# Performance work log

Measured on AMD Instinct MI355X. Metric: run time of the kernel, lower is better.

The kernel has to match this reference:

```python
import jax, jax.numpy as jnp
import numpy as np

D = 1024      # embed_dim
H = 1365      # expert_hidden_dim = int(4096 / (select_top_k + num_shared_experts)) = int(4096/3)
E = 7         # num_experts = base_num_experts*factor - num_shared = 8 - 1
K = 2         # select_top_k
S_EXP = 1     # num_shared_experts
ALPHA = 0.01
C_Z = 0.001


def setup_inputs() -> dict:
    key = jax.random.key(0)
    ks = jax.random.split(key, 8)
    scaled = lambda k, shape, fan: jax.random.normal(k, shape, jnp.float32) * (1.0 / np.sqrt(fan))
    return {
        "x": jax.random.normal(ks[0], (4, 512, D), jnp.float32),
        "Wg": scaled(ks[1], (E, D), D),            # router weight (no bias)
        "W1": scaled(ks[2], (E, H, D), D),          # routed experts ffn[0] weight
        "b1": jnp.zeros((E, H), jnp.float32),
        "W2": scaled(ks[3], (E, D, H), H),          # routed experts ffn[3] weight
        "b2": jnp.zeros((E, D), jnp.float32),
        "Ws1": scaled(ks[4], (S_EXP, H, D), D),     # shared experts
        "bs1": jnp.zeros((S_EXP, H), jnp.float32),
        "Ws2": scaled(ks[5], (S_EXP, D, H), H),
        "bs2": jnp.zeros((S_EXP, D), jnp.float32),
    }


def _moe_forward(x, Wg, W1, b1, W2, b2, Ws1, bs1, Ws2, bs2):
    B, S, _ = x.shape
    xf = x.reshape(-1, D)                               # [N, D] flattened tokens
    N = xf.shape[0]

    # Gate (eval mode: no router noise, no dropout)
    logits = jnp.einsum('nd,ed->ne', xf, Wg)            # [N, E]
    dense_gate = jax.nn.softmax(logits, axis=-1)
    topk_logits, topk_idx = jax.lax.top_k(logits, K)    # [N, K]
    topk_w = jax.nn.softmax(topk_logits, axis=-1)       # [N, K]

    # Dense gate matrix: weight for selected experts, 0 elsewhere (equivalent to
    # the sorted dispatch + per-expert FFN + index_add combine in the original).
    gates = jnp.zeros((N, E), xf.dtype).at[jnp.arange(N)[:, None], topk_idx].set(topk_w)

    # Routed experts: exact GELU (approximate='none')
    h = jax.nn.gelu(jnp.einsum('nd,ehd->enh', xf, W1) + b1[:, None, :], approximate=False)  # [E, N, H]
    y = jnp.einsum('enh,edh->end', h, W2) + b2[:, None, :]                                  # [E, N, D]
    routed = jnp.einsum('ne,end->nd', gates, y)                                             # [N, D]

    # Shared experts (applied to every token, summed)
    hs = jax.nn.gelu(jnp.einsum('nd,shd->snh', xf, Ws1) + bs1[:, None, :], approximate=False)
    shared = jnp.einsum('snh,sdh->nd', hs, Ws2) + bs2.sum(0)

    final = (routed + shared).reshape(B, S, D)

    # Aux losses
    counts = jnp.zeros((E,), jnp.float32).at[topk_idx.reshape(-1)].add(1.0)  # bincount (non-diff, like torch long)
    dispatch_fraction = jax.lax.stop_gradient(counts) / (N * K)
    l_aux = ALPHA * E * jnp.sum(dispatch_fraction * dense_gate.mean(axis=0))
    cz_lz = C_Z * jnp.mean(jax.nn.logsumexp(logits, axis=-1) ** 2)
    return final, l_aux, cz_lz


def reference(x, Wg, W1, b1, W2, b2, Ws1, bs1, Ws2, bs2):
    return _moe_forward(x, Wg, W1, b1, W2, b2, Ws1, bs1, Ws2, bs2)
```

## Files before the change

kernel.cpp:

```cpp
#include <hip/hip_runtime.h>
#include <hip/hip_bf16.h>
#include <math.h>

typedef unsigned short u16;
typedef __attribute__((ext_vector_type(8))) short bf16x8;
typedef __attribute__((ext_vector_type(16))) float f32x16;

constexpr int D_ = 1024;
constexpr int H_ = 1365;
constexpr int E_ = 7;
constexpr int NTOK = 2048;
constexpr int HP = 1408;
constexpr int NE = 8;
constexpr int SHARED_BASE = 4096;
constexpr int SLOTS = 6144;

#define CI_COUNT 0
#define CI_OFF   8

constexpr size_t WS_CTRL = 0;
constexpr size_t WS_TIDX = 256;
constexpr size_t WS_TW   = WS_TIDX + (size_t)NTOK*2*4;
constexpr size_t WS_PROB = WS_TW   + (size_t)NTOK*2*4;
constexpr size_t WS_LSE2 = WS_PROB + (size_t)NTOK*8*4;
constexpr size_t WS_STOK = WS_LSE2 + (size_t)NTOK*4;
constexpr size_t WS_SW   = WS_STOK + (size_t)SLOTS*4;
constexpr size_t WS_B1   = WS_SW   + (size_t)SLOTS*4;
constexpr size_t WS_B2   = WS_B1   + (size_t)NE*H_*4;
constexpr size_t WS_XB   = ((WS_B2 + (size_t)NE*D_*4) + 255) & ~(size_t)255;
constexpr size_t WS_W1B  = WS_XB  + (size_t)NTOK*D_*2;
constexpr size_t WS_W2B  = WS_W1B + (size_t)NE*H_*D_*2;
constexpr size_t WS_HEB  = WS_W2B + (size_t)NE*D_*HP*2;

__device__ __forceinline__ u16 f2bf(float f) {
    __hip_bfloat16 h = __float2bfloat16(f);
    return __builtin_bit_cast(u16, h);
}

__device__ __forceinline__ void gload_lds16(const u16* g, u16* l) {
    __builtin_amdgcn_global_load_lds(
        (const __attribute__((address_space(1))) void*)g,
        (__attribute__((address_space(3))) void*)l, 16, 0, 0);
}

__device__ __forceinline__ uint4 pack8(float4 a, float4 b) {
    union { u16 h[8]; uint4 v; } u;
    u.h[0]=f2bf(a.x); u.h[1]=f2bf(a.y); u.h[2]=f2bf(a.z); u.h[3]=f2bf(a.w);
    u.h[4]=f2bf(b.x); u.h[5]=f2bf(b.y); u.h[6]=f2bf(b.z); u.h[7]=f2bf(b.w);
    return u.v;
}

__device__ __forceinline__ float fast_gelu(float v) {
    float u = 0.7978845608f * v * (1.f + 0.044715f * v * v);
    float e = __expf(2.f * u);
    float t = 1.f - 2.f / (e + 1.f);
    return 0.5f * v * (1.f + t);
}

#define BM 128
#define BN 128
#define KSTEP 64
#define ATILE (BM*KSTEP)

#define MFMA32(a,b,c) __builtin_amdgcn_mfma_f32_32x32x16_bf16(a, b, c, 0, 0, 0)

template<bool USE_STOK>
__device__ __forceinline__ void gemm1_body(u16* As, u16* Bs,
    const u16* xb, const u16* w1e, const float* b1e,
    const int* stok, int offset, int m0, int valid, int nt,
    u16* heb)
{
    int t = threadIdx.x, wid = t >> 6, lane = t & 63;
    int rl = lane >> 3, cl = lane & 7;
    int sg = cl ^ rl;

    const u16* aP[2]; const u16* bP[2]; int dOff[2];
    #pragma unroll
    for (int c = 0; c < 2; c++) {
        int row = wid*16 + c*8 + rl;
        int ar = min(row, valid-1);
        int tok = USE_STOK ? stok[offset + m0 + ar] : (m0 + ar);
        aP[c] = xb + (size_t)tok*D_ + sg*8;
        int jg = min(nt*BN + row, H_-1);
        bP[c] = w1e + (size_t)jg*D_ + sg*8;
        dOff[c] = (wid*16 + c*8)*KSTEP;
    }

    int wm = (wid >> 2)*64, wn = (wid & 3)*32;
    int fr = lane & 31, hi = lane >> 5, f7 = lane & 7;
    f32x16 acc[2] = {};

    #pragma unroll
    for (int c = 0; c < 2; c++) {
        gload_lds16(aP[c], As + dOff[c]);
        gload_lds16(bP[c], Bs + dOff[c]);
    }
    constexpr int nIter = D_/KSTEP;
    int cur = 0;
    for (int tt = 0; tt < nIter; ++tt) {
        if (tt + 1 < nIter) {
            int bo2 = (cur^1)*ATILE;
            int ko = (tt+1)*KSTEP;
            #pragma unroll
            for (int c = 0; c < 2; c++) {
                gload_lds16(aP[c]+ko, As + bo2 + dOff[c]);
                gload_lds16(bP[c]+ko, Bs + bo2 + dOff[c]);
            }
            asm volatile("s_waitcnt vmcnt(4)" ::: "memory");
        } else {
            asm volatile("s_waitcnt vmcnt(0)" ::: "memory");
        }
        __builtin_amdgcn_s_barrier();
        __builtin_amdgcn_sched_barrier(0);
        const u16* ab = As + cur*ATILE;
        const u16* bb = Bs + cur*ATILE;
        __builtin_amdgcn_s_setprio(1);
        #pragma unroll
        for (int ks = 0; ks < 4; ks++) {
            int ch = ((ks*2 + hi) ^ f7) * 8;
            bf16x8 a0 = *(const bf16x8*)&ab[(wm +      fr)*KSTEP + ch];
            bf16x8 a1 = *(const bf16x8*)&ab[(wm + 32 + fr)*KSTEP + ch];
            bf16x8 b0 = *(const bf16x8*)&bb[(wn +      fr)*KSTEP + ch];
            acc[0] = MFMA32(a0, b0, acc[0]);
            acc[1] = MFMA32(a1, b0, acc[1]);
        }
        __builtin_amdgcn_s_setprio(0);
        asm volatile("s_waitcnt lgkmcnt(0)" ::: "memory");
        __builtin_amdgcn_sched_barrier(0);
        __builtin_amdgcn_s_barrier();
        cur ^= 1;
    }

    int gcol = nt*BN + wn + fr;
    bool cok = gcol < H_;
    float bias = cok ? b1e[gcol] : 0.f;
    #pragma unroll
    for (int mf = 0; mf < 2; mf++) {
        #pragma unroll
        for (int r = 0; r < 16; r++) {
            int row = wm + mf*32 + (r & 3) + 8*(r >> 2) + 4*hi;
            if (row < valid) {
                float v = 0.f;
                if (cok) v = fast_gelu(acc[mf][r] + bias);
                heb[(size_t)(offset + m0 + row)*HP + gcol] = f2bf(v);
            }
        }
    }
}

template<int MODE>
__device__ __forceinline__ void gemm2_body(u16* As, u16* Bs,
    const u16* heb, const u16* w2e, const float* b2e, const float* sw,
    int offset, int m0, int valid, int nt, float* out, const int* stok)
{
    int t = threadIdx.x, wid = t >> 6, lane = t & 63;
    int rl = lane >> 3, cl = lane & 7;
    int sg = cl ^ rl;

    const u16* aP[2]; const u16* bP[2]; int dOff[2];
    #pragma unroll
    for (int c = 0; c < 2; c++) {
        int row = wid*16 + c*8 + rl;
        int ar = min(row, valid-1);
        aP[c] = heb + (size_t)(offset + m0 + ar)*HP + sg*8;
        int jg = nt*BN + row;
        bP[c] = w2e + (size_t)jg*HP + sg*8;
        dOff[c] = (wid*16 + c*8)*KSTEP;
    }

    int wm = (wid >> 2)*64, wn = (wid & 3)*32;
    int fr = lane & 31, hi = lane >> 5, f7 = lane & 7;
    f32x16 acc[2] = {};

    #pragma unroll
    for (int c = 0; c < 2; c++) {
        gload_lds16(aP[c], As + dOff[c]);
        gload_lds16(bP[c], Bs + dOff[c]);
    }
    constexpr int nIter = HP/KSTEP;
    int cur = 0;
    for (int tt = 0; tt < nIter; ++tt) {
        if (tt + 1 < nIter) {
            int bo2 = (cur^1)*ATILE;
            int ko = (tt+1)*KSTEP;
            #pragma unroll
            for (int c = 0; c < 2; c++) {
                gload_lds16(aP[c]+ko, As + bo2 + dOff[c]);
                gload_lds16(bP[c]+ko, Bs + bo2 + dOff[c]);
            }
            asm volatile("s_waitcnt vmcnt(4)" ::: "memory");
        } else {
            asm volatile("s_waitcnt vmcnt(0)" ::: "memory");
        }
        __builtin_amdgcn_s_barrier();
        __builtin_amdgcn_sched_barrier(0);
        const u16* ab = As + cur*ATILE;
        const u16* bb = Bs + cur*ATILE;
        __builtin_amdgcn_s_setprio(1);
        #pragma unroll
        for (int ks = 0; ks < 4; ks++) {
            int ch = ((ks*2 + hi) ^ f7) * 8;
            bf16x8 a0 = *(const bf16x8*)&ab[(wm +      fr)*KSTEP + ch];
            bf16x8 a1 = *(const bf16x8*)&ab[(wm + 32 + fr)*KSTEP + ch];
            bf16x8 b0 = *(const bf16x8*)&bb[(wn +      fr)*KSTEP + ch];
            acc[0] = MFMA32(a0, b0, acc[0]);
            acc[1] = MFMA32(a1, b0, acc[1]);
        }
        __builtin_amdgcn_s_setprio(0);
        asm volatile("s_waitcnt lgkmcnt(0)" ::: "memory");
        __builtin_amdgcn_sched_barrier(0);
        __builtin_amdgcn_s_barrier();
        cur ^= 1;
    }

    int gcol = nt*BN + wn + fr;
    float bias = b2e[gcol];
    #pragma unroll
    for (int mf = 0; mf < 2; mf++) {
        #pragma unroll
        for (int r = 0; r < 16; r++) {
            int row = wm + mf*32 + (r & 3) + 8*(r >> 2) + 4*hi;
            if (row < valid) {
                if (MODE == 0) {
                    out[(size_t)(m0 + row)*D_ + gcol] = acc[mf][r] + bias;
                } else {
                    int slot = offset + m0 + row;
                    atomicAdd(out + (size_t)stok[slot]*D_ + gcol,
                              sw[slot]*(acc[mf][r] + bias));
                }
            }
        }
    }
}

__device__ void finalize_body(char* smem,
    const int* tidx, const float* tw, const float* probs, const float* lse2,
    int* ci, int* stok, float* sw, float* out)
{
    int*   lt   = (int*)smem;
    float* psum = (float*)(smem + 16384);
    float* lsum = (float*)(smem + 16384 + 32);
    int*   cntS = (int*)(smem + 16448);
    int*   offS = (int*)(smem + 16480);
    int t = threadIdx.x;
    if (t < 8) { psum[t] = 0.f; cntS[t] = 0; }
    if (t == 0) *lsum = 0.f;
    for (int i = t; i < NTOK*2; i += 512) lt[i] = tidx[i];
    __syncthreads();
    float lp[E_] = {}; float ll = 0.f;
    for (int n = t; n < NTOK; n += 512) {
        #pragma unroll
        for (int e = 0; e < E_; e++) lp[e] += probs[n*8+e];
        ll += lse2[n];
    }
    #pragma unroll
    for (int e = 0; e < E_; e++) atomicAdd(&psum[e], lp[e]);
    atomicAdd(lsum, ll);
    int wid = t >> 6, lane = t & 63;
    if (wid < 7) {
        int c = 0;
        for (int i = lane; i < NTOK*2; i += 64) c += (lt[i] == wid) ? 1 : 0;
        #pragma unroll
        for (int m = 32; m >= 1; m >>= 1) c += __shfl_xor(c, m);
        if (lane == 0) cntS[wid] = c;
    } else {
        for (int n = lane; n < NTOK; n += 64) {
            stok[SHARED_BASE+n] = n; sw[SHARED_BASE+n] = 1.f;
        }
    }
    __syncthreads();
    if (t == 0) {
        int o = 0;
        for (int e = 0; e < E_; e++) { offS[e] = o; o += cntS[e]; }
        offS[7] = SHARED_BASE; cntS[7] = NTOK;
        float la = 0.f;
        for (int e = 0; e < E_; e++)
            la += ((float)cntS[e] / (float)(NTOK*2)) * (psum[e] / (float)NTOK);
        out[(size_t)NTOK*D_]     = 0.01f * 7.f * la;
        out[(size_t)NTOK*D_ + 1] = 0.001f * (*lsum) / (float)NTOK;
        #pragma unroll
        for (int e = 0; e < 8; e++) { ci[CI_COUNT+e] = cntS[e]; ci[CI_OFF+e] = offS[e]; }
    }
    __syncthreads();
    if (wid < 7) {
        int base = offS[wid], run = 0;
        for (int c0 = 0; c0 < NTOK*2; c0 += 64) {
            bool m = (lt[c0 + lane] == wid);
            unsigned long long bal = __ballot(m);
            int pre = __popcll(bal & ((1ull << lane) - 1ull));
            if (m) {
                int i = c0 + lane;
                int s = base + run + pre;
                stok[s] = i >> 1; sw[s] = tw[i];
            }
            run += __popcll(bal);
        }
    }
}

__global__ void prep_kernel(
    const float* __restrict__ x, const float* __restrict__ Wg,
    const float* __restrict__ W1, const float* __restrict__ Ws1,
    const float* __restrict__ b1, const float* __restrict__ bs1,
    int* __restrict__ tidx, float* __restrict__ tw,
    float* __restrict__ probs, float* __restrict__ lse2,
    u16* __restrict__ xb, u16* __restrict__ w1b, float* __restrict__ b1all)
{
    int b = blockIdx.x;
    if (b < 512) {
        int wid = threadIdx.x >> 6, lane = threadIdx.x & 63;
        int n = b*4 + wid;
        float p[E_] = {};
        const float* xr = x + (size_t)n*D_;
        u16* xbr = xb + (size_t)n*D_;
        #pragma unroll
        for (int j = 0; j < 4; j++) {
            int d0 = lane*4 + j*256;
            float4 xv = *(const float4*)(xr + d0);
            ushort4 h;
            h.x = f2bf(xv.x); h.y = f2bf(xv.y); h.z = f2bf(xv.z); h.w = f2bf(xv.w);
            *(ushort4*)(xbr + d0) = h;
            #pragma unroll
            for (int e = 0; e < E_; e++) {
                float4 wv = *(const float4*)(Wg + e*D_ + d0);
                p[e] += xv.x*wv.x + xv.y*wv.y + xv.z*wv.z + xv.w*wv.w;
            }
        }
        #pragma unroll
        for (int e = 0; e < E_; e++) {
            float v = p[e];
            #pragma unroll
            for (int m = 32; m >= 1; m >>= 1) v += __shfl_xor(v, m);
            p[e] = v;
        }
        if (lane == 0) {
            float mx = p[0];
            #pragma unroll
            for (int e = 1; e < E_; e++) mx = fmaxf(mx, p[e]);
            float pr[E_], sum = 0.f;
            #pragma unroll
            for (int e = 0; e < E_; e++) { pr[e] = __expf(p[e]-mx); sum += pr[e]; }
            float lse = mx + logf(sum);
            int i0 = 0;
            #pragma unroll
            for (int e = 1; e < E_; e++) if (p[e] > p[i0]) i0 = e;
            int i1 = -1;
            #pragma unroll
            for (int e = 0; e < E_; e++) if (e != i0 && (i1 < 0 || p[e] > p[i1])) i1 = e;
            float g = expf(p[i1] - p[i0]);
            tidx[n*2] = i0; tidx[n*2+1] = i1;
            tw[n*2] = 1.f/(1.f+g); tw[n*2+1] = g/(1.f+g);
            float inv = 1.f/sum;
            #pragma unroll
            for (int e = 0; e < E_; e++) probs[n*8+e] = pr[e]*inv;
            lse2[n] = lse*lse;
        }
        return;
    }
    const unsigned G1 = (unsigned)(NE*H_*D_/8);
    const unsigned W1FLAT = 7u*(unsigned)(H_*D_);
    const unsigned total = G1 + (unsigned)(NE*H_);
    const unsigned stride = 1024u*256u;
    for (unsigned i = (unsigned)(b-512)*256u + threadIdx.x; i < total; i += stride) {
        if (i < G1) {
            unsigned base = i*8u;
            const float* src = (base < W1FLAT) ? (W1 + base) : (Ws1 + (base - W1FLAT));
            const float4* s = (const float4*)src;
            ((uint4*)w1b)[i] = pack8(s[0], s[1]);
        } else {
            unsigned k = i - G1;
            unsigned e = k / 1365u, j = k - e*1365u;
            b1all[k] = (e < 7u) ? b1[k] : bs1[j];
        }
    }
}

__global__ __launch_bounds__(512, 4) void k2_kernel(
    const float* __restrict__ W2, const float* __restrict__ Ws2,
    const float* __restrict__ b2, const float* __restrict__ bs2,
    u16* __restrict__ w2b, float* __restrict__ b2all,
    const int* __restrict__ tidx, const float* __restrict__ tw,
    const float* __restrict__ probs, const float* __restrict__ lse2,
    int* __restrict__ ci, int* __restrict__ stok, float* __restrict__ sw,
    float* __restrict__ out,
    const u16* __restrict__ xb, const u16* __restrict__ w1b,
    const float* __restrict__ b1all, u16* __restrict__ heb)
{
    __shared__ u16 As[2*ATILE];
    __shared__ u16 Bs[2*ATILE];
    int b = blockIdx.x;
    if (b == 0) {
        finalize_body((char*)As, tidx, tw, probs, lse2, ci, stok, sw, out);
        return;
    }
    if (b <= 176) {
        int tdx = b - 1;
        int mt = tdx/11, nt = tdx - mt*11;
        gemm1_body<false>(As, Bs, xb, w1b + (size_t)7*H_*D_, b1all + 7*H_,
                          nullptr, SHARED_BASE, mt*BM, BM, nt, heb);
        return;
    }
    const unsigned DH  = (unsigned)(D_*H_);
    const unsigned G2v = 2u*DH;
    const unsigned BIAS = (unsigned)(NE*D_/4);
    const unsigned PAD  = (unsigned)(NE*D_)*(unsigned)(HP-H_);
    const unsigned total = G2v + BIAS + PAD;
    const unsigned stride = 832u*512u;
    for (unsigned g = (unsigned)(b-177)*512u + threadIdx.x; g < total; g += stride) {
        if (g < G2v) {
            unsigned base = g*4u;
            unsigned ec = base / DH;
            unsigned r  = base - ec*DH;
            unsigned drow = r / 1365u;
            unsigned h  = r - drow*1365u;
            const float* src = (ec < 7u) ? (W2 + base) : (Ws2 + (base - 7u*DH));
            float4 v = *(const float4*)src;
            float vv[4] = {v.x, v.y, v.z, v.w};
            u16* rb = w2b + ((size_t)ec*D_ + drow)*HP;
            if (h + 3u < 1365u) {
                #pragma unroll
                for (int q = 0; q < 4; q++) rb[h+q] = f2bf(vv[q]);
            } else {
                #pragma unroll
                for (int q = 0; q < 4; q++) {
                    unsigned hq = h + q, dr = 0;
                    if (hq >= 1365u) { hq -= 1365u; dr = 1; }
                    rb[(size_t)dr*HP + hq] = f2bf(vv[q]);
                }
            }
            continue;
        }
        unsigned k = g - G2v;
        if (k < BIAS) {
            unsigned base = k*4u;
            unsigned e = base >> 10, j = base & 1023u;
            float4 v = (e < 7u) ? *(const float4*)(b2 + base) : *(const float4*)(bs2 + j);
            *(float4*)(b2all + base) = v;
            continue;
        }
        k -= BIAS;
        unsigned row = k / 43u, j = k - row*43u;
        w2b[(size_t)row*HP + 1365u + j] = 0;
    }
}

__global__ __launch_bounds__(512, 4) void k3_kernel(
    const int* __restrict__ ci, const int* __restrict__ stok,
    const u16* __restrict__ xb, const u16* __restrict__ w1b,
    const float* __restrict__ b1all, u16* __restrict__ heb,
    const u16* __restrict__ w2b, const float* __restrict__ b2all,
    float* __restrict__ out)
{
    __shared__ u16 As[2*ATILE];
    __shared__ u16 Bs[2*ATILE];
    int x = blockIdx.x, yb = blockIdx.y;
    if (yb < 176) {
        if (x == 7) return;
        int e = x, mt = yb/11, nt = yb - mt*11;
        int count = ci[CI_COUNT+e];
        int m0 = mt*BM;
        if (m0 >= count) return;
        gemm1_body<true>(As, Bs, xb, w1b + (size_t)e*H_*D_, b1all + e*H_,
                         stok, ci[CI_OFF+e], m0, min(BM, count-m0), nt, heb);
    } else {
        int idx = (yb - 176)*8 + x;
        int mt = idx >> 3, nt = idx & 7;
        gemm2_body<0>(As, Bs, heb, w2b + (size_t)7*D_*HP, b2all + 7*D_,
                      nullptr, SHARED_BASE, mt*BM, BM, nt, out, nullptr);
    }
}

__global__ __launch_bounds__(512, 4) void k4_kernel(
    const int* __restrict__ ci, const int* __restrict__ stok, const float* __restrict__ sw,
    const u16* __restrict__ heb, const u16* __restrict__ w2b,
    const float* __restrict__ b2all, float* __restrict__ out)
{
    __shared__ u16 As[2*ATILE];
    __shared__ u16 Bs[2*ATILE];
    int x = blockIdx.x;
    if (x == 7) return;
    int yb = blockIdx.y;
    int e = x, mt = yb >> 3, nt = yb & 7;
    int count = ci[CI_COUNT+e];
    int m0 = mt*BM;
    if (m0 >= count) return;
    gemm2_body<1>(As, Bs, heb, w2b + (size_t)e*D_*HP, b2all + e*D_,
                  sw, ci[CI_OFF+e], m0, min(BM, count-m0), nt, out, stok);
}

extern "C" void kernel_launch(void* const* d_in, const int* in_sizes, int n_in,
                              void* d_out, int out_size, void* d_ws, size_t ws_size,
                              hipStream_t stream)
{
    const float* x   = (const float*)d_in[0];
    const float* Wg  = (const float*)d_in[1];
    const float* W1  = (const float*)d_in[2];
    const float* b1  = (const float*)d_in[3];
    const float* W2  = (const float*)d_in[4];
    const float* b2  = (const float*)d_in[5];
    const float* Ws1 = (const float*)d_in[6];
    const float* bs1 = (const float*)d_in[7];
    const float* Ws2 = (const float*)d_in[8];
    const float* bs2 = (const float*)d_in[9];
    float* out = (float*)d_out;
    char* ws = (char*)d_ws;

    int*   ci    = (int*)(ws + WS_CTRL);
    int*   tidx  = (int*)(ws + WS_TIDX);
    float* tw    = (float*)(ws + WS_TW);
    float* probs = (float*)(ws + WS_PROB);
    float* lse2  = (float*)(ws + WS_LSE2);
    int*   stok  = (int*)(ws + WS_STOK);
    float* sw    = (float*)(ws + WS_SW);
    float* b1all = (float*)(ws + WS_B1);
    float* b2all = (float*)(ws + WS_B2);
    u16*   xb    = (u16*)(ws + WS_XB);
    u16*   w1b   = (u16*)(ws + WS_W1B);
    u16*   w2b   = (u16*)(ws + WS_W2B);
    u16*   heb   = (u16*)(ws + WS_HEB);

    prep_kernel<<<1536, 256, 0, stream>>>(x, Wg, W1, Ws1, b1, bs1,
                                          tidx, tw, probs, lse2, xb, w1b, b1all);
    k2_kernel<<<1009, 512, 0, stream>>>(W2, Ws2, b2, bs2, w2b, b2all,
                                        tidx, tw, probs, lse2, ci, stok, sw, out,
                                        xb, w1b, b1all, heb);
    k3_kernel<<<dim3(8, 176 + 16), 512, 0, stream>>>(ci, stok, xb, w1b, b1all, heb,
                                                     w2b, b2all, out);
    k4_kernel<<<dim3(8, 128), 512, 0, stream>>>(ci, stok, sw, heb, w2b, b2all, out);
}
```

Baseline: 140.3 us.

## Switch to 16x16 MFMA, single-buffer LDS, and raise occupancy to 8 blocks

Replaces the 32x32x16 MFMA tiling with 16x16x32 bf16 MFMAs (4x2 fragments per wave) and drops the double-buffered LDS pipeline in favour of a single buffer with syncthreads around each load. This halves shared memory per block, and launch bounds are raised to 8 blocks per CU to increase occupancy. The finalize routine is adapted to use the two smaller LDS arrays. In exchange, loads are no longer overlapped with compute within a block, so latency hiding now relies on other resident blocks.

```diff
diff --git a/kernel.cpp b/kernel.cpp
--- a/kernel.cpp
+++ b/kernel.cpp
@@ -4,7 +4,7 @@
 
 typedef unsigned short u16;
 typedef __attribute__((ext_vector_type(8))) short bf16x8;
-typedef __attribute__((ext_vector_type(16))) float f32x16;
+typedef __attribute__((ext_vector_type(4))) float f32x4;
 
 constexpr int D_ = 1024;
 constexpr int H_ = 1365;
@@ -62,7 +62,7 @@
 #define KSTEP 64
 #define ATILE (BM*KSTEP)
 
-#define MFMA32(a,b,c) __builtin_amdgcn_mfma_f32_32x32x16_bf16(a, b, c, 0, 0, 0)
+#define MFMA16(a,b,c) __builtin_amdgcn_mfma_f32_16x16x32_bf16(a, b, c, 0, 0, 0)
 
 template<bool USE_STOK>
 __device__ __forceinline__ void gemm1_body(u16* As, u16* Bs,
@@ -87,62 +87,55 @@
     }
 
     int wm = (wid >> 2)*64, wn = (wid & 3)*32;
-    int fr = lane & 31, hi = lane >> 5, f7 = lane & 7;
-    f32x16 acc[2] = {};
-
+    int frow = lane & 15, kgrp = lane >> 4, swz = frow & 7;
+    f32x4 acc[4][2] = {};
+
+    constexpr int nIter = D_/KSTEP;
+    for (int tt = 0; tt < nIter; ++tt) {
+        __syncthreads();
+        int ko = tt*KSTEP;
+        #pragma unroll
+        for (int c = 0; c < 2; c++) {
+            gload_lds16(aP[c]+ko, As + dOff[c]);
+            gload_lds16(bP[c]+ko, Bs + dOff[c]);
+        }
+        __syncthreads();
+        __builtin_amdgcn_s_setprio(1);
+        #pragma unroll
+        for (int s = 0; s < 2; s++) {
+            int cc = ((s*4 + kgrp) ^ swz) * 8;
+            bf16x8 af[4], bf[2];
+            #pragma unroll
+            for (int mf = 0; mf < 4; mf++)
+                af[mf] = *(const bf16x8*)&As[(wm + mf*16 + frow)*KSTEP + cc];
+            #pragma unroll
+            for (int nf = 0; nf < 2; nf++)
+                bf[nf] = *(const bf16x8*)&Bs[(wn + nf*16 + frow)*KSTEP + cc];
+            #pragma unroll
+            for (int mf = 0; mf < 4; mf++)
+                #pragma unroll
+                for (int nf = 0; nf < 2; nf++)
+                    acc[mf][nf] = MFMA16(af[mf], bf[nf], acc[mf][nf]);
+        }
+        __builtin_amdgcn_s_setprio(0);
+    }
+
+    int r4 = (lane >> 4)*4, cEl = lane & 15;
     #pragma unroll
-    for (int c = 0; c < 2; c++) {
-        gload_lds16(aP[c], As + dOff[c]);
-        gload_lds16(bP[c], Bs + dOff[c]);
-    }
-    constexpr int nIter = D_/KSTEP;
-    int cur = 0;
-    for (int tt = 0; tt < nIter; ++tt) {
-        if (tt + 1 < nIter) {
-            int bo2 = (cur^1)*ATILE;
-            int ko = (tt+1)*KSTEP;
-            #pragma unroll
-            for (int c = 0; c < 2; c++) {
-                gload_lds16(aP[c]+ko, As + bo2 + dOff[c]);
-                gload_lds16(bP[c]+ko, Bs + bo2 + dOff[c]);
-            }
-            asm volatile("s_waitcnt vmcnt(4)" ::: "memory");
-        } else {
-            asm volatile("s_waitcnt vmcnt(0)" ::: "memory");
-        }
-        __builtin_amdgcn_s_barrier();
-        __builtin_amdgcn_sched_barrier(0);
-        const u16* ab = As + cur*ATILE;
-        const u16* bb = Bs + cur*ATILE;
-        __builtin_amdgcn_s_setprio(1);
-        #pragma unroll
-        for (int ks = 0; ks < 4; ks++) {
-            int ch = ((ks*2 + hi) ^ f7) * 8;
-            bf16x8 a0 = *(const bf16x8*)&ab[(wm +      fr)*KSTEP + ch];
-            bf16x8 a1 = *(const bf16x8*)&ab[(wm + 32 + fr)*KSTEP + ch];
-            bf16x8 b0 = *(const bf16x8*)&bb[(wn +      fr)*KSTEP + ch];
-            acc[0] = MFMA32(a0, b0, acc[0]);
-            acc[1] = MFMA32(a1, b0, acc[1]);
-        }
-        __builtin_amdgcn_s_setprio(0);
-        asm volatile("s_waitcnt lgkmcnt(0)" ::: "memory");
-        __builtin_amdgcn_sched_barrier(0);
-        __builtin_amdgcn_s_barrier();
-        cur ^= 1;
-    }
-
-    int gcol = nt*BN + wn + fr;
-    bool cok = gcol < H_;
-    float bias = cok ? b1e[gcol] : 0.f;
-    #pragma unroll
-    for (int mf = 0; mf < 2; mf++) {
-        #pragma unroll
-        for (int r = 0; r < 16; r++) {
-            int row = wm + mf*32 + (r & 3) + 8*(r >> 2) + 4*hi;
-            if (row < valid) {
-                float v = 0.f;
-                if (cok) v = fast_gelu(acc[mf][r] + bias);
-                heb[(size_t)(offset + m0 + row)*HP + gcol] = f2bf(v);
+    for (int nf = 0; nf < 2; nf++) {
+        int gcol = nt*BN + wn + nf*16 + cEl;
+        bool cok = gcol < H_;
+        float bias = cok ? b1e[gcol] : 0.f;
+        #pragma unroll
+        for (int mf = 0; mf < 4; mf++) {
+            #pragma unroll
+            for (int r = 0; r < 4; r++) {
+                int row = wm + mf*16 + r4 + r;
+                if (row < valid) {
+                    float v = 0.f;
+                    if (cok) v = fast_gelu(acc[mf][nf][r] + bias);
+                    heb[(size_t)(offset + m0 + row)*HP + gcol] = f2bf(v);
+                }
             }
         }
     }
@@ -169,79 +162,72 @@
     }
 
     int wm = (wid >> 2)*64, wn = (wid & 3)*32;
-    int fr = lane & 31, hi = lane >> 5, f7 = lane & 7;
-    f32x16 acc[2] = {};
-
+    int frow = lane & 15, kgrp = lane >> 4, swz = frow & 7;
+    f32x4 acc[4][2] = {};
+
+    constexpr int nIter = HP/KSTEP;
+    for (int tt = 0; tt < nIter; ++tt) {
+        __syncthreads();
+        int ko = tt*KSTEP;
+        #pragma unroll
+        for (int c = 0; c < 2; c++) {
+            gload_lds16(aP[c]+ko, As + dOff[c]);
+            gload_lds16(bP[c]+ko, Bs + dOff[c]);
+        }
+        __syncthreads();
+        __builtin_amdgcn_s_setprio(1);
+        #pragma unroll
+        for (int s = 0; s < 2; s++) {
+            int cc = ((s*4 + kgrp) ^ swz) * 8;
+            bf16x8 af[4], bf[2];
+            #pragma unroll
+            for (int mf = 0; mf < 4; mf++)
+                af[mf] = *(const bf16x8*)&As[(wm + mf*16 + frow)*KSTEP + cc];
+            #pragma unroll
+            for (int nf = 0; nf < 2; nf++)
+                bf[nf] = *(const bf16x8*)&Bs[(wn + nf*16 + frow)*KSTEP + cc];
+            #pragma unroll
+            for (int mf = 0; mf < 4; mf++)
+                #pragma unroll
+                for (int nf = 0; nf < 2; nf++)
+                    acc[mf][nf] = MFMA16(af[mf], bf[nf], acc[mf][nf]);
+        }
+        __builtin_amdgcn_s_setprio(0);
+    }
+
+    int r4 = (lane >> 4)*4, cEl = lane & 15;
     #pragma unroll
-    for (int c = 0; c < 2; c++) {
-        gload_lds16(aP[c], As + dOff[c]);
-        gload_lds16(bP[c], Bs + dOff[c]);
-    }
-    constexpr int nIter = HP/KSTEP;
-    int cur = 0;
-    for (int tt = 0; tt < nIter; ++tt) {
-        if (tt + 1 < nIter) {
-            int bo2 = (cur^1)*ATILE;
-            int ko = (tt+1)*KSTEP;
-            #pragma unroll
-            for (int c = 0; c < 2; c++) {
-                gload_lds16(aP[c]+ko, As + bo2 + dOff[c]);
-                gload_lds16(bP[c]+ko, Bs + bo2 + dOff[c]);
-            }
-            asm volatile("s_waitcnt vmcnt(4)" ::: "memory");
-        } else {
-            asm volatile("s_waitcnt vmcnt(0)" ::: "memory");
-        }
-        __builtin_amdgcn_s_barrier();
-        __builtin_amdgcn_sched_barrier(0);
-        const u16* ab = As + cur*ATILE;
-        const u16* bb = Bs + cur*ATILE;
-        __builtin_amdgcn_s_setprio(1);
-        #pragma unroll
-        for (int ks = 0; ks < 4; ks++) {
-            int ch = ((ks*2 + hi) ^ f7) * 8;
-            bf16x8 a0 = *(const bf16x8*)&ab[(wm +      fr)*KSTEP + ch];
-            bf16x8 a1 = *(const bf16x8*)&ab[(wm + 32 + fr)*KSTEP + ch];
-            bf16x8 b0 = *(const bf16x8*)&bb[(wn +      fr)*KSTEP + ch];
-            acc[0] = MFMA32(a0, b0, acc[0]);
-            acc[1] = MFMA32(a1, b0, acc[1]);
-        }
-        __builtin_amdgcn_s_setprio(0);
-        asm volatile("s_waitcnt lgkmcnt(0)" ::: "memory");
-        __builtin_amdgcn_sched_barrier(0);
-        __builtin_amdgcn_s_barrier();
-        cur ^= 1;
-    }
-
-    int gcol = nt*BN + wn + fr;
-    float bias = b2e[gcol];
-    #pragma unroll
-    for (int mf = 0; mf < 2; mf++) {
-        #pragma unroll
-        for (int r = 0; r < 16; r++) {
-            int row = wm + mf*32 + (r & 3) + 8*(r >> 2) + 4*hi;
-            if (row < valid) {
-                if (MODE == 0) {
-                    out[(size_t)(m0 + row)*D_ + gcol] = acc[mf][r] + bias;
-                } else {
-                    int slot = offset + m0 + row;
-                    atomicAdd(out + (size_t)stok[slot]*D_ + gcol,
-                              sw[slot]*(acc[mf][r] + bias));
+    for (int nf = 0; nf < 2; nf++) {
+        int gcol = nt*BN + wn + nf*16 + cEl;
+        float bias = b2e[gcol];
+        #pragma unroll
+        for (int mf = 0; mf < 4; mf++) {
+            #pragma unroll
+            for (int r = 0; r < 4; r++) {
+                int row = wm + mf*16 + r4 + r;
+                if (row < valid) {
+                    if (MODE == 0) {
+                        out[(size_t)(m0 + row)*D_ + gcol] = acc[mf][nf][r] + bias;
+                    } else {
+                        int slot = offset + m0 + row;
+                        atomicAdd(out + (size_t)stok[slot]*D_ + gcol,
+                                  sw[slot]*(acc[mf][nf][r] + bias));
+                    }
                 }
             }
         }
     }
 }
 
-__device__ void finalize_body(char* smem,
+__device__ void finalize_body(char* big, char* small,
     const int* tidx, const float* tw, const float* probs, const float* lse2,
     int* ci, int* stok, float* sw, float* out)
 {
-    int*   lt   = (int*)smem;
-    float* psum = (float*)(smem + 16384);
-    float* lsum = (float*)(smem + 16384 + 32);
-    int*   cntS = (int*)(smem + 16448);
-    int*   offS = (int*)(smem + 16480);
+    int*   lt   = (int*)big;
+    float* psum = (float*)small;
+    float* lsum = (float*)(small + 32);
+    int*   cntS = (int*)(small + 64);
+    int*   offS = (int*)(small + 96);
     int t = threadIdx.x;
     if (t < 8) { psum[t] = 0.f; cntS[t] = 0; }
     if (t == 0) *lsum = 0.f;
@@ -375,7 +361,7 @@
     }
 }
 
-__global__ __launch_bounds__(512, 4) void k2_kernel(
+__global__ __launch_bounds__(512, 8) void k2_kernel(
     const float* __restrict__ W2, const float* __restrict__ Ws2,
     const float* __restrict__ b2, const float* __restrict__ bs2,
     u16* __restrict__ w2b, float* __restrict__ b2all,
@@ -386,11 +372,11 @@
     const u16* __restrict__ xb, const u16* __restrict__ w1b,
     const float* __restrict__ b1all, u16* __restrict__ heb)
 {
-    __shared__ u16 As[2*ATILE];
-    __shared__ u16 Bs[2*ATILE];
+    __shared__ u16 As[ATILE];
+    __shared__ u16 Bs[ATILE];
     int b = blockIdx.x;
     if (b == 0) {
-        finalize_body((char*)As, tidx, tw, probs, lse2, ci, stok, sw, out);
+        finalize_body((char*)As, (char*)Bs, tidx, tw, probs, lse2, ci, stok, sw, out);
         return;
     }
     if (b <= 176) {
@@ -444,15 +430,15 @@
     }
 }
 
-__global__ __launch_bounds__(512, 4) void k3_kernel(
+__global__ __launch_bounds__(512, 8) void k3_kernel(
     const int* __restrict__ ci, const int* __restrict__ stok,
     const u16* __restrict__ xb, const u16* __restrict__ w1b,
     const float* __restrict__ b1all, u16* __restrict__ heb,
     const u16* __restrict__ w2b, const float* __restrict__ b2all,
     float* __restrict__ out)
 {
-    __shared__ u16 As[2*ATILE];
-    __shared__ u16 Bs[2*ATILE];
+    __shared__ u16 As[ATILE];
+    __shared__ u16 Bs[ATILE];
     int x = blockIdx.x, yb = blockIdx.y;
     if (yb < 176) {
         if (x == 7) return;
@@ -470,13 +456,13 @@
     }
 }
 
-__global__ __launch_bounds__(512, 4) void k4_kernel(
+__global__ __launch_bounds__(512, 8) void k4_kernel(
     const int* __restrict__ ci, const int* __restrict__ stok, const float* __restrict__ sw,
     const u16* __restrict__ heb, const u16* __restrict__ w2b,
     const float* __restrict__ b2all, float* __restrict__ out)
 {
-    __shared__ u16 As[2*ATILE];
-    __shared__ u16 Bs[2*ATILE];
+    __shared__ u16 As[ATILE];
+    __shared__ u16 Bs[ATILE];
     int x = blockIdx.x;
     if (x == 7) return;
     int yb = blockIdx.y;
```

Result: faster. 134.8 us (-4.0%).
